# Performance work log

Hardware: AMD Instinct MI355X
Metric: run time of the kernel (lower is better)

The kernel has to match this reference:

```python
import jax, jax.numpy as jnp
import numpy as np

DECAY = 0.99
EPS = 1e-05
B, C, H, W = 64, 64, 64, 64   # C == embedding_dim
K = 512                       # num_embedding


def setup_inputs() -> dict:
    key = jax.random.key(0)
    k1, k2 = jax.random.split(key)
    inp = jax.random.normal(k1, (B, C, H, W), dtype=jnp.float32)
    embedding = jax.random.normal(k2, (C, K), dtype=jnp.float32)
    cluster_size = jnp.zeros((K,), dtype=jnp.float32)
    embedding_avg = embedding  # buffer initialized as a clone of embedding
    return {"input": inp, "embedding": embedding,
            "cluster_size": cluster_size, "embedding_avg": embedding_avg}


def reference(input, embedding, cluster_size, embedding_avg):
    # NCHW -> NHWC, flatten to [N, C]
    x = jnp.transpose(input, (0, 2, 3, 1))           # [B,H,W,C]
    flat = x.reshape(-1, embedding.shape[0])          # [N,C]
    # squared L2 distances to all K codes: [N,K]
    dist = (jnp.sum(flat * flat, axis=1, keepdims=True)
            - 2.0 * flat @ embedding
            + jnp.sum(embedding * embedding, axis=0, keepdims=True))
    ind = jnp.argmin(dist, axis=1)                    # [N] int
    # gather codes (uses OLD embedding, as in torch)
    quantize = jnp.take(embedding.T, ind, axis=0).reshape(x.shape)  # [B,H,W,C]
    # EMA updates (training branch). Avoid materializing one-hot:
    counts = jnp.zeros((K,), dtype=flat.dtype).at[ind].add(1.0)      # onehot.sum(0)
    embedding_sum = jax.ops.segment_sum(flat, ind, num_segments=K).T  # [C,K] == flat.T @ onehot
    new_cluster_size = cluster_size * DECAY + (1.0 - DECAY) * counts
    new_embedding_avg = embedding_avg * DECAY + (1.0 - DECAY) * embedding_sum
    n = jnp.sum(new_cluster_size)
    cs = (new_cluster_size + EPS) / (n + K * EPS) * n
    new_embedding = new_embedding_avg / cs[None, :]
    # commitment loss and straight-through estimator
    diff = jnp.mean((jax.lax.stop_gradient(quantize) - x) ** 2)
    quantize_st = x + jax.lax.stop_gradient(quantize - x)
    out = jnp.transpose(quantize_st, (0, 3, 1, 2))    # back to NCHW
    embedding_ind = ind.reshape(x.shape[:-1])         # [B,H,W]
    return out, diff, embedding_ind, new_embedding, new_cluster_size, new_embedding_avg
```

## Files before the change

kernel.cpp:

```cpp
#include <hip/hip_runtime.h>
#include <cstdint>
#include <cstddef>

typedef _Float16 half4v __attribute__((ext_vector_type(4)));
typedef _Float16 half8v __attribute__((ext_vector_type(8)));
typedef float    f32x4  __attribute__((ext_vector_type(4)));

#define N_PTS   262144
#define CDIM    64
#define KCODES  512
#define TAUA    5e-3f
#define FLAG_CAP 65536u
#define STATS_WGS 256

#define OFF_DIFF 16777216u
#define OFF_IND  16777217u
#define OFF_EMB  17039361u
#define OFF_CSZ  17072129u
#define OFF_AVG  17072641u

__global__ __launch_bounds__(512) void k_main(
    const float* __restrict__ in, const float* __restrict__ emb,
    float* __restrict__ out,
    int* __restrict__ ind_buf, float* __restrict__ diff_acc,
    unsigned* __restrict__ nflag, int* __restrict__ flaglist)
{
    __shared__ __align__(16) char bsm[133120];
    float* ee2_lds = (float*)(bsm + 131072);
    const int tid = threadIdx.x;

    {
        const int col = tid;
        const int xr  = (col & 7) << 4;
        float s = 0.f;
        #pragma unroll
        for (int c0 = 0; c0 < CDIM; c0 += 4) {
            float v[4];
            #pragma unroll
            for (int i = 0; i < 4; ++i) v[i] = emb[(c0 + i)*KCODES + col];
            half4v h, lo;
            #pragma unroll
            for (int i = 0; i < 4; ++i) {
                s = fmaf(v[i], v[i], s);
                _Float16 hh = (_Float16)v[i];
                h[i]  = hh;
                lo[i] = (_Float16)(v[i] - (float)hh);
            }
            const int wb = col*128 + ((c0*2) ^ xr);
            *(half4v*)(bsm + wb)         = h;
            *(half4v*)(bsm + 65536 + wb) = lo;
        }
        ee2_lds[col] = 0.5f * s;
    }
    __syncthreads();

    const int w  = tid >> 6, l = tid & 63;
    const int g  = l >> 4,  lc = l & 15;

    for (int r = 0; r < 2; ++r) {
        const int pbase = (blockIdx.x << 10) + (r << 9) + (w << 6);
        const int b     = pbase >> 12;
        const float* inb = in + ((size_t)b << 18) + ((pbase & 4095) + lc);

        half8v ah[4][2], al[4][2];
        float xs = 0.f;
        #pragma unroll
        for (int t = 0; t < 4; ++t)
            #pragma unroll
            for (int s = 0; s < 2; ++s)
                #pragma unroll
                for (int j = 0; j < 8; ++j) {
                    const int c = s*32 + g*8 + j;
                    const float x = inb[(size_t)c*4096 + t*16];
                    xs = fmaf(x, x, xs);
                    const float xf = -x;
                    const _Float16 hh = (_Float16)xf;
                    ah[t][s][j] = hh;
                    al[t][s][j] = (_Float16)(xf - (float)hh);
                }

        float d1[4][4], d2[4][4]; int k1[4][4];
        #pragma unroll
        for (int t = 0; t < 4; ++t)
            #pragma unroll
            for (int rr = 0; rr < 4; ++rr) { d1[t][rr] = 3.4e38f; d2[t][rr] = 3.4e38f; k1[t][rr] = 0; }

        for (int ct = 0; ct < 32; ++ct) {
            const int col  = (ct << 4) + lc;
            const float sd = ee2_lds[col];
            const int rb   = col*128 + ((g*16) ^ ((col & 7) << 4));
            half8v bh0 = *(const half8v*)(bsm + rb);
            half8v bh1 = *(const half8v*)(bsm + (rb ^ 64));
            half8v bl0 = *(const half8v*)(bsm + 65536 + rb);
            half8v bl1 = *(const half8v*)(bsm + 65536 + (rb ^ 64));

            #pragma unroll
            for (int t = 0; t < 4; ++t) {
                f32x4 acc0 = {sd, sd, sd, sd};
                f32x4 acc1 = {0.f, 0.f, 0.f, 0.f};
                acc0 = __builtin_amdgcn_mfma_f32_16x16x32_f16(al[t][0], bh0, acc0, 0, 0, 0);
                acc1 = __builtin_amdgcn_mfma_f32_16x16x32_f16(al[t][1], bh1, acc1, 0, 0, 0);
                acc0 = __builtin_amdgcn_mfma_f32_16x16x32_f16(ah[t][0], bl0, acc0, 0, 0, 0);
                acc1 = __builtin_amdgcn_mfma_f32_16x16x32_f16(ah[t][1], bl1, acc1, 0, 0, 0);
                acc0 = __builtin_amdgcn_mfma_f32_16x16x32_f16(ah[t][0], bh0, acc0, 0, 0, 0);
                acc1 = __builtin_amdgcn_mfma_f32_16x16x32_f16(ah[t][1], bh1, acc1, 0, 0, 0);
                #pragma unroll
                for (int rr = 0; rr < 4; ++rr) {
                    const float d = acc0[rr] + acc1[rr];
                    const bool cc = d < d1[t][rr];
                    d2[t][rr] = fminf(d2[t][rr], fmaxf(d, d1[t][rr]));
                    d1[t][rr] = fminf(d1[t][rr], d);
                    k1[t][rr] = cc ? col : k1[t][rr];
                }
            }
        }

        #pragma unroll
        for (int m = 1; m <= 8; m <<= 1) {
            #pragma unroll
            for (int t = 0; t < 4; ++t)
                #pragma unroll
                for (int rr = 0; rr < 4; ++rr) {
                    const float od1 = __shfl_xor(d1[t][rr], m);
                    const int   ok1 = __shfl_xor(k1[t][rr], m);
                    const float od2 = __shfl_xor(d2[t][rr], m);
                    const float nd2 = fminf(fmaxf(d1[t][rr], od1), fminf(d2[t][rr], od2));
                    const bool take = (od1 < d1[t][rr]) || (od1 == d1[t][rr] && ok1 < k1[t][rr]);
                    d1[t][rr] = take ? od1 : d1[t][rr];
                    k1[t][rr] = take ? ok1 : k1[t][rr];
                    d2[t][rr] = nd2;
                }
        }

        float ds = 0.f;
        if (lc == 0) {
            #pragma unroll
            for (int t = 0; t < 4; ++t) {
                const int nb = pbase + t*16 + (g << 2);
                int4 iv = make_int4(k1[t][0], k1[t][1], k1[t][2], k1[t][3]);
                *(int4*)(ind_buf + nb) = iv;
                #pragma unroll
                for (int rr = 0; rr < 4; ++rr) {
                    out[OFF_IND + nb + rr] = (float)k1[t][rr];
                    ds += d1[t][rr];
                    if (d2[t][rr] - d1[t][rr] < TAUA) {
                        unsigned ix = atomicAdd(nflag, 1u);
                        if (ix < FLAG_CAP) flaglist[ix] = nb + rr;
                    }
                }
            }
        }
        #pragma unroll
        for (int m = 1; m < 64; m <<= 1) {
            ds += __shfl_xor(ds, m);
            xs += __shfl_xor(xs, m);
        }
        if (l == 0) atomicAdd(diff_acc, 2.f*ds + xs);
    }
}

__global__ void k_refine(const float* __restrict__ in, const float* __restrict__ emb,
                         const unsigned* __restrict__ nflag, const int* __restrict__ flaglist,
                         int* __restrict__ ind_buf, float* __restrict__ out)
{
    const int gtid = blockIdx.x*blockDim.x + threadIdx.x;
    const int wid  = gtid >> 6;
    const int lane = threadIdx.x & 63;
    const int nw   = (gridDim.x * blockDim.x) >> 6;
    unsigned nf = *nflag; if (nf > FLAG_CAP) nf = FLAG_CAP;
    for (unsigned f = wid; f < nf; f += nw) {
        const int n = flaglist[f];
        const int b = n >> 12, hw = n & 4095;
        const float* xb = in + ((size_t)b << 18) + hw;
        const float* er = emb + lane*8;
        double dd[8] = {0,0,0,0,0,0,0,0};
        for (int c = 0; c < CDIM; ++c) {
            const double xv = (double)xb[(size_t)c << 12];
            #pragma unroll
            for (int j = 0; j < 8; ++j) {
                double t = xv - (double)er[c*KCODES + j];
                dd[j] = fma(t, t, dd[j]);
            }
        }
        double bd = 1e300; int bk = 0;
        #pragma unroll
        for (int j = 0; j < 8; ++j) {
            const int kk = lane*8 + j;
            if (dd[j] < bd) { bd = dd[j]; bk = kk; }
        }
        for (int off = 32; off; off >>= 1) {
            double od = __shfl_xor(bd, off);
            int    ok = __shfl_xor(bk, off);
            if (od < bd || (od == bd && ok < bk)) { bd = od; bk = ok; }
        }
        if (lane == 0) { ind_buf[n] = bk; out[OFF_IND + n] = (float)bk; }
    }
}

__global__ __launch_bounds__(512) void k_tail(const float* __restrict__ in,
    const float* __restrict__ emb, const int* __restrict__ ind_buf,
    float* __restrict__ p_sum, float* __restrict__ p_cnt, float* __restrict__ out)
{
    __shared__ __align__(16) char xsm[2][CDIM*128];
    __shared__ int   ind_lds[2][32];
    __shared__ float s_cnt[KCODES];

    const int tid = threadIdx.x;

    if (blockIdx.x >= STATS_WGS) {
        const int gid = (blockIdx.x - STATS_WGS)*512 + tid;
        const int i  = gid << 2;
        const int hw = i & 4095;
        const int c  = (i >> 12) & 63;
        const int b  = i >> 18;
        const int n  = (b << 12) + hw;
        const int4 iv = *(const int4*)(ind_buf + n);
        const float* er = emb + (c << 9);
        float4 o = make_float4(er[iv.x], er[iv.y], er[iv.z], er[iv.w]);
        *(float4*)(out + i) = o;
        return;
    }

    const int wg  = blockIdx.x;
    const int n0  = wg << 10;
    const int b   = n0 >> 12;
    const float* inb = in + ((size_t)b << 18) + (n0 & 4095);

    for (int i = tid; i < KCODES; i += 512) s_cnt[i] = 0.f;

    const int sc  = tid >> 3;
    const int sp  = (tid & 7) << 2;
    const int sxr = (sc & 7) << 4;
    const int wb_hi = sc*128 + ((sp*2) ^ sxr);

    const int w  = tid >> 6, l = tid & 63;
    const int g  = l >> 4,  lc = l & 15;
    const int k0w = w << 6;

    f32x4 acc[4][4];
    #pragma unroll
    for (int ci = 0; ci < 4; ++ci)
        #pragma unroll
        for (int kt = 0; kt < 4; ++kt) acc[ci][kt] = (f32x4){0.f, 0.f, 0.f, 0.f};

    {
        const float4 xv = *(const float4*)(inb + (size_t)sc*4096 + sp);
        half4v h;
        #pragma unroll
        for (int i = 0; i < 4; ++i) h[i] = (_Float16)(((const float*)&xv)[i]);
        *(half4v*)(&xsm[0][0] + wb_hi) = h;
        if (tid < 8) *(int4*)&ind_lds[0][tid*4] = *(const int4*)(ind_buf + n0 + tid*4);
    }

    for (int t = 0; t < 32; ++t) {
        __syncthreads();
        float4 nxt; int4 niv;
        if (t < 31) {
            nxt = *(const float4*)(inb + (size_t)sc*4096 + (t+1)*32 + sp);
            if (tid < 8) niv = *(const int4*)(ind_buf + n0 + (t+1)*32 + tid*4);
        }
        if (tid < 32) atomicAdd(&s_cnt[ind_lds[t & 1][tid]], 1.f);

        const char* xb = &xsm[t & 1][0];
        half8v ah[4];
        #pragma unroll
        for (int ci = 0; ci < 4; ++ci) {
            const int c  = (ci << 4) + lc;
            const int xr = (c & 7) << 4;
            ah[ci] = *(const half8v*)(xb + c*128 + ((g*16) ^ xr));
        }
        int idv[8];
        *(int4*)&idv[0] = *(const int4*)&ind_lds[t & 1][g*8];
        *(int4*)&idv[4] = *(const int4*)&ind_lds[t & 1][g*8 + 4];
        #pragma unroll
        for (int kt = 0; kt < 4; ++kt) {
            const int tgt = k0w + (kt << 4) + lc;
            half8v bf;
            #pragma unroll
            for (int j = 0; j < 8; ++j) bf[j] = (idv[j] == tgt) ? (_Float16)1.0f : (_Float16)0.0f;
            #pragma unroll
            for (int ci = 0; ci < 4; ++ci)
                acc[ci][kt] = __builtin_amdgcn_mfma_f32_16x16x32_f16(ah[ci], bf, acc[ci][kt], 0, 0, 0);
        }
        if (t < 31) {
            half4v h;
            #pragma unroll
            for (int i = 0; i < 4; ++i) h[i] = (_Float16)(((const float*)&nxt)[i]);
            *(half4v*)(&xsm[(t+1) & 1][0] + wb_hi) = h;
            if (tid < 8) *(int4*)&ind_lds[(t+1) & 1][tid*4] = niv;
        }
    }
    __syncthreads();

    float* ps = p_sum + (size_t)wg * (CDIM*KCODES);
    #pragma unroll
    for (int ci = 0; ci < 4; ++ci)
        #pragma unroll
        for (int kt = 0; kt < 4; ++kt)
            #pragma unroll
            for (int rr = 0; rr < 4; ++rr)
                ps[((ci << 4) + (g << 2) + rr)*KCODES + k0w + (kt << 4) + lc] = acc[ci][kt][rr];
    float* pc = p_cnt + wg * KCODES;
    for (int i = tid; i < KCODES; i += 512) pc[i] = s_cnt[i];
}

__global__ __launch_bounds__(256) void k_reduce1(const float* __restrict__ p_sum,
    const float* __restrict__ p_cnt, float* __restrict__ partial8,
    float* __restrict__ cnt8, int wsl)
{
    const int ic = blockIdx.x & 31, ws = blockIdx.x >> 5;
    const int i4 = ic*1024 + threadIdx.x*4;
    const float* base = p_sum + (size_t)ws*wsl*(CDIM*KCODES) + i4;
    float4 s = make_float4(0.f, 0.f, 0.f, 0.f);
    for (int w = 0; w < wsl; ++w) {
        const float4 v = *(const float4*)(base + (size_t)w*(CDIM*KCODES));
        s.x += v.x; s.y += v.y; s.z += v.z; s.w += v.w;
    }
    *(float4*)(partial8 + ws*(CDIM*KCODES) + i4) = s;
    if (ic == 0) {
        for (int k = threadIdx.x; k < KCODES; k += 256) {
            float c = 0.f;
            for (int w = 0; w < wsl; ++w) c += p_cnt[(ws*wsl + w)*KCODES + k];
            cnt8[ws*KCODES + k] = c;
        }
    }
}

__global__ __launch_bounds__(512) void k_final(const float* __restrict__ partial8,
    const float* __restrict__ cnt8, const float* __restrict__ csz,
    const float* __restrict__ eavg, const float* __restrict__ diff_acc,
    float* __restrict__ out)
{
    __shared__ float red[512];
    __shared__ float cs_lds[512];
    const int k = threadIdx.x;
    float c = 0.f;
    #pragma unroll
    for (int p = 0; p < 8; ++p) c += cnt8[p*KCODES + k];
    const float ncs = csz[k]*0.99f + 0.01f*c;
    if (blockIdx.x == 0) out[OFF_CSZ + k] = ncs;
    red[k] = ncs;
    __syncthreads();
    for (int s = 256; s > 0; s >>= 1) { if (k < s) red[k] += red[k+s]; __syncthreads(); }
    const float n = red[0];
    cs_lds[k] = (ncs + 1e-5f) / (n + 0.00512f) * n;
    if (blockIdx.x == 0 && k == 0) out[OFF_DIFF] = diff_acc[0] * (1.f/16777216.f);
    __syncthreads();
    if (k < 256) {
        const int i = (blockIdx.x*256 + k)*4;
        float4 s4 = make_float4(0.f, 0.f, 0.f, 0.f);
        #pragma unroll
        for (int p = 0; p < 8; ++p) {
            const float4 v = *(const float4*)(partial8 + p*(CDIM*KCODES) + i);
            s4.x += v.x; s4.y += v.y; s4.z += v.z; s4.w += v.w;
        }
        const float4 ea = *(const float4*)(eavg + i);
        const float a0 = ea.x*0.99f + 0.01f*s4.x;
        const float a1 = ea.y*0.99f + 0.01f*s4.y;
        const float a2 = ea.z*0.99f + 0.01f*s4.z;
        const float a3 = ea.w*0.99f + 0.01f*s4.w;
        const int kb = i & (KCODES-1);
        out[OFF_AVG + i]     = a0;  out[OFF_AVG + i + 1] = a1;
        out[OFF_AVG + i + 2] = a2;  out[OFF_AVG + i + 3] = a3;
        out[OFF_EMB + i]     = a0 / cs_lds[kb];
        out[OFF_EMB + i + 1] = a1 / cs_lds[kb + 1];
        out[OFF_EMB + i + 2] = a2 / cs_lds[kb + 2];
        out[OFF_EMB + i + 3] = a3 / cs_lds[kb + 3];
    }
}

extern "C" void kernel_launch(void* const* d_in, const int* in_sizes, int n_in,
                              void* d_out, int out_size, void* d_ws, size_t ws_size,
                              hipStream_t stream)
{
    const float* in   = (const float*)d_in[0];
    const float* emb  = (const float*)d_in[1];
    const float* csz  = (const float*)d_in[2];
    const float* eavg = (const float*)d_in[3];
    float* out = (float*)d_out;
    char* ws = (char*)d_ws;

    int*      ind      = (int*)(ws + 2048);
    float*    diff_acc = (float*)(ws + 1050624);
    unsigned* nflag    = (unsigned*)(ws + 1050640);
    int*      flaglist = (int*)(ws + 1050656);
    const size_t off_part = 1447968;
    const int swgs = STATS_WGS;
    float* p_sum    = (float*)(ws + off_part);
    float* p_cnt    = (float*)(ws + off_part + (size_t)swgs*(CDIM*KCODES)*4);
    float* partial8 = (float*)(ws + off_part + (size_t)swgs*133120);
    float* cnt8     = (float*)(ws + off_part + (size_t)swgs*133120 + 1048576);

    hipMemsetAsync(ws + 1050624, 0, 32, stream);

    hipLaunchKernelGGL(k_main,    dim3(256),        dim3(512), 0, stream, in, emb, out, ind, diff_acc, nflag, flaglist);
    hipLaunchKernelGGL(k_refine,  dim3(256),        dim3(256), 0, stream, in, emb, nflag, flaglist, ind, out);
    hipLaunchKernelGGL(k_tail,    dim3(STATS_WGS + 8192), dim3(512), 0, stream, in, emb, ind, p_sum, p_cnt, out);
    hipLaunchKernelGGL(k_reduce1, dim3(256),        dim3(256), 0, stream, p_sum, p_cnt, partial8, cnt8, swgs >> 3);
    hipLaunchKernelGGL(k_final,   dim3(32),         dim3(512), 0, stream, partial8, cnt8, csz, eavg, diff_acc, out);
}
```

Baseline: 197.1 us.

## Merge two-stage partial reduction into final kernel and move index output to tail

Removes the intermediate reduce kernel. The final kernel, with 32 workgroups, now sums all 256 per-workgroup partial sums and counts directly. The float copy of the index output moves from k_main and k_refine into the gather part of k_tail, so it is written once, after refinement. This saves a launch and an intermediate buffer round trip, but each of the 32 workgroups now streams 256 partials serially, which exposes far less parallelism for the 32 MB reduction.

```diff
diff --git a/kernel.cpp b/kernel.cpp
--- a/kernel.cpp
+++ b/kernel.cpp
@@ -141,7 +141,6 @@
                 *(int4*)(ind_buf + nb) = iv;
                 #pragma unroll
                 for (int rr = 0; rr < 4; ++rr) {
-                    out[OFF_IND + nb + rr] = (float)k1[t][rr];
                     ds += d1[t][rr];
                     if (d2[t][rr] - d1[t][rr] < TAUA) {
                         unsigned ix = atomicAdd(nflag, 1u);
@@ -161,7 +160,7 @@
 
 __global__ void k_refine(const float* __restrict__ in, const float* __restrict__ emb,
                          const unsigned* __restrict__ nflag, const int* __restrict__ flaglist,
-                         int* __restrict__ ind_buf, float* __restrict__ out)
+                         int* __restrict__ ind_buf)
 {
     const int gtid = blockIdx.x*blockDim.x + threadIdx.x;
     const int wid  = gtid >> 6;
@@ -193,7 +192,7 @@
             int    ok = __shfl_xor(bk, off);
             if (od < bd || (od == bd && ok < bk)) { bd = od; bk = ok; }
         }
-        if (lane == 0) { ind_buf[n] = bk; out[OFF_IND + n] = (float)bk; }
+        if (lane == 0) ind_buf[n] = bk;
     }
 }
 
@@ -218,6 +217,12 @@
         const float* er = emb + (c << 9);
         float4 o = make_float4(er[iv.x], er[iv.y], er[iv.z], er[iv.w]);
         *(float4*)(out + i) = o;
+        if (c == 0) {
+            out[OFF_IND + n]     = (float)iv.x;
+            out[OFF_IND + n + 1] = (float)iv.y;
+            out[OFF_IND + n + 2] = (float)iv.z;
+            out[OFF_IND + n + 3] = (float)iv.w;
+        }
         return;
     }
 
@@ -304,30 +309,8 @@
     for (int i = tid; i < KCODES; i += 512) pc[i] = s_cnt[i];
 }
 
-__global__ __launch_bounds__(256) void k_reduce1(const float* __restrict__ p_sum,
-    const float* __restrict__ p_cnt, float* __restrict__ partial8,
-    float* __restrict__ cnt8, int wsl)
-{
-    const int ic = blockIdx.x & 31, ws = blockIdx.x >> 5;
-    const int i4 = ic*1024 + threadIdx.x*4;
-    const float* base = p_sum + (size_t)ws*wsl*(CDIM*KCODES) + i4;
-    float4 s = make_float4(0.f, 0.f, 0.f, 0.f);
-    for (int w = 0; w < wsl; ++w) {
-        const float4 v = *(const float4*)(base + (size_t)w*(CDIM*KCODES));
-        s.x += v.x; s.y += v.y; s.z += v.z; s.w += v.w;
-    }
-    *(float4*)(partial8 + ws*(CDIM*KCODES) + i4) = s;
-    if (ic == 0) {
-        for (int k = threadIdx.x; k < KCODES; k += 256) {
-            float c = 0.f;
-            for (int w = 0; w < wsl; ++w) c += p_cnt[(ws*wsl + w)*KCODES + k];
-            cnt8[ws*KCODES + k] = c;
-        }
-    }
-}
-
-__global__ __launch_bounds__(512) void k_final(const float* __restrict__ partial8,
-    const float* __restrict__ cnt8, const float* __restrict__ csz,
+__global__ __launch_bounds__(512) void k_last(const float* __restrict__ p_sum,
+    const float* __restrict__ p_cnt, const float* __restrict__ csz,
     const float* __restrict__ eavg, const float* __restrict__ diff_acc,
     float* __restrict__ out)
 {
@@ -335,8 +318,7 @@
     __shared__ float cs_lds[512];
     const int k = threadIdx.x;
     float c = 0.f;
-    #pragma unroll
-    for (int p = 0; p < 8; ++p) c += cnt8[p*KCODES + k];
+    for (int w = 0; w < STATS_WGS; ++w) c += p_cnt[w*KCODES + k];
     const float ncs = csz[k]*0.99f + 0.01f*c;
     if (blockIdx.x == 0) out[OFF_CSZ + k] = ncs;
     red[k] = ncs;
@@ -347,11 +329,10 @@
     if (blockIdx.x == 0 && k == 0) out[OFF_DIFF] = diff_acc[0] * (1.f/16777216.f);
     __syncthreads();
     if (k < 256) {
-        const int i = (blockIdx.x*256 + k)*4;
+        const int i = blockIdx.x*1024 + k*4;
         float4 s4 = make_float4(0.f, 0.f, 0.f, 0.f);
-        #pragma unroll
-        for (int p = 0; p < 8; ++p) {
-            const float4 v = *(const float4*)(partial8 + p*(CDIM*KCODES) + i);
+        for (int w = 0; w < STATS_WGS; ++w) {
+            const float4 v = *(const float4*)(p_sum + (size_t)w*(CDIM*KCODES) + i);
             s4.x += v.x; s4.y += v.y; s4.z += v.z; s4.w += v.w;
         }
         const float4 ea = *(const float4*)(eavg + i);
@@ -386,16 +367,13 @@
     int*      flaglist = (int*)(ws + 1050656);
     const size_t off_part = 1447968;
     const int swgs = STATS_WGS;
-    float* p_sum    = (float*)(ws + off_part);
-    float* p_cnt    = (float*)(ws + off_part + (size_t)swgs*(CDIM*KCODES)*4);
-    float* partial8 = (float*)(ws + off_part + (size_t)swgs*133120);
-    float* cnt8     = (float*)(ws + off_part + (size_t)swgs*133120 + 1048576);
+    float* p_sum = (float*)(ws + off_part);
+    float* p_cnt = (float*)(ws + off_part + (size_t)swgs*(CDIM*KCODES)*4);
 
     hipMemsetAsync(ws + 1050624, 0, 32, stream);
 
-    hipLaunchKernelGGL(k_main,    dim3(256),        dim3(512), 0, stream, in, emb, out, ind, diff_acc, nflag, flaglist);
-    hipLaunchKernelGGL(k_refine,  dim3(256),        dim3(256), 0, stream, in, emb, nflag, flaglist, ind, out);
-    hipLaunchKernelGGL(k_tail,    dim3(STATS_WGS + 8192), dim3(512), 0, stream, in, emb, ind, p_sum, p_cnt, out);
-    hipLaunchKernelGGL(k_reduce1, dim3(256),        dim3(256), 0, stream, p_sum, p_cnt, partial8, cnt8, swgs >> 3);
-    hipLaunchKernelGGL(k_final,   dim3(32),         dim3(512), 0, stream, partial8, cnt8, csz, eavg, diff_acc, out);
-}
+    hipLaunchKernelGGL(k_main,   dim3(256),              dim3(512), 0, stream, in, emb, out, ind, diff_acc, nflag, flaglist);
+    hipLaunchKernelGGL(k_refine, dim3(256),              dim3(256), 0, stream, in, emb, nflag, flaglist, ind);
+    hipLaunchKernelGGL(k_tail,   dim3(STATS_WGS + 8192), dim3(512), 0, stream, in, emb, ind, p_sum, p_cnt, out);
+    hipLaunchKernelGGL(k_last,   dim3(32),               dim3(512), 0, stream, p_sum, p_cnt, csz, eavg, diff_acc, out);
+}
```

Result: no change. 194.1 us (-1.5%).
